# Kernel optimization log

Hardware: AMD Instinct MI355X
Metric: run time of the kernel (lower is better)

## Reference

```python
import jax, jax.numpy as jnp
import numpy as np

BATCH = 2048
INPUT_DIM = 512
N = 8 ** 4  # reservoir_n ** reservoir_d = 4096
T = 16
NEG_SLOPE = 0.1
SPARSITY = 0.1  # fraction of nonzero entries in the pre-trained reservoir W


def setup_inputs() -> dict:
    key = jax.random.key(0)
    kx, kw, km = jax.random.split(key, 3)
    x = jax.random.normal(kx, (BATCH, INPUT_DIM), dtype=jnp.float32)
    # Sparse pre-trained reservoir weights; scale keeps spectral norm ~O(1)
    # so the T-step recurrence neither explodes nor vanishes.
    mask = (jax.random.uniform(km, (N, N)) < SPARSITY).astype(jnp.float32)
    W = jax.random.normal(kw, (N, N), dtype=jnp.float32) * mask / jnp.sqrt(SPARSITY * N)
    return {"x": x, "W": W}


def reference(x, W):
    # Pad input [B, input_dim] -> initial state S [B, N]
    S0 = jnp.pad(x, ((0, 0), (0, N - x.shape[1])))

    def step(S, _):
        S = jax.nn.leaky_relu(S @ W, negative_slope=NEG_SLOPE)
        return S, None

    S_final, _ = jax.lax.scan(step, S0, None, length=T)
    return S_final
```

## Files before the change

kernel.cpp:

```cpp
#include <hip/hip_runtime.h>


#define BATCH 2048
#define NDIM  4096
#define INDIM 512
#define BM 128
#define BN 128
#define BK 32

typedef _Float16 f16x8 __attribute__((ext_vector_type(8)));
typedef float    f32x4 __attribute__((ext_vector_type(4)));

__device__ __forceinline__ void async16(const void* gsrc, void* ldst) {
  const __attribute__((address_space(1))) unsigned int* g =
      (const __attribute__((address_space(1))) unsigned int*)gsrc;
  __attribute__((address_space(3))) unsigned int* l =
      (__attribute__((address_space(3))) unsigned int*)ldst;
  __builtin_amdgcn_global_load_lds(g, l, 16, 0, 0);
}

__device__ __forceinline__ f16x8 frag(const _Float16* s, int row, int q) {
  int ch = q ^ ((row >> 1) & 3);
  return *(const f16x8*)(s + row * BK + ch * 8);
}

__global__ void prep_x(const float* __restrict__ x,
                       _Float16* __restrict__ Sh, _Float16* __restrict__ Sl) {
  size_t i = (size_t)blockIdx.x * 256 + threadIdx.x;
  int b = (int)(i >> 12);
  int n = (int)(i & (NDIM - 1));
  float v = (n < INDIM) ? x[(size_t)b * INDIM + n] : 0.0f;
  _Float16 h = (_Float16)v;
  Sh[i] = h;
  Sl[i] = (_Float16)(v - (float)h);
}

__global__ void prep_w(const float* __restrict__ W,
                       _Float16* __restrict__ Wth, _Float16* __restrict__ Wtl) {
  __shared__ float tile[32][33];
  int k0 = blockIdx.y * 32, n0 = blockIdx.x * 32;
  int tx = threadIdx.x, ty = threadIdx.y;
  for (int r = 0; r < 4; r++) {
    int k = k0 + ty + r * 8;
    tile[ty + r * 8][tx] = W[(size_t)k * NDIM + n0 + tx];
  }
  __syncthreads();
  for (int r = 0; r < 4; r++) {
    int n = n0 + ty + r * 8;
    float v = tile[tx][ty + r * 8] * 256.0f;
    _Float16 h = (_Float16)v;
    Wth[(size_t)n * NDIM + k0 + tx] = h;
    Wtl[(size_t)n * NDIM + k0 + tx] = (_Float16)(v - (float)h);
  }
}

template <int MODE>
__global__ __launch_bounds__(256, 2) void step_kernel(
    const _Float16* __restrict__ Ah, const _Float16* __restrict__ Al,
    const _Float16* __restrict__ Bh, const _Float16* __restrict__ Bl,
    _Float16* __restrict__ Dh, _Float16* __restrict__ Dl,
    float* __restrict__ Dout, int k_len) {
  __shared__ _Float16 sAh[BM * BK];
  __shared__ _Float16 sAl[BM * BK];
  __shared__ _Float16 sBh[BN * BK];
  __shared__ _Float16 sBl[BN * BK];

  const int tid = threadIdx.x;
  const int lane = tid & 63;
  const int w = tid >> 6;
  const int wm = w >> 1;
  const int wn = w & 1;
  const int bm = blockIdx.y * BM;
  const int bn = blockIdx.x * BN;

  const int sr = lane >> 2;
  const int cl = lane & 3;
  const int fm = lane & 15;
  const int fq = lane >> 4;

  f32x4 acc[4][4];
  for (int i = 0; i < 4; i++)
    for (int j = 0; j < 4; j++) acc[i][j] = (f32x4){0.f, 0.f, 0.f, 0.f};

  for (int kt = 0; kt < k_len; kt += BK) {
    for (int q = 0; q < 2; q++) {
      int t = w * 2 + q;
      int r = t * 16 + sr;
      int cg = cl ^ ((r >> 1) & 3);
      size_t goA = (size_t)(bm + r) * NDIM + kt + cg * 8;
      size_t goB = (size_t)(bn + r) * NDIM + kt + cg * 8;
      int lo = r * BK + cl * 8;
      async16(Ah + goA, sAh + lo);
      async16(Al + goA, sAl + lo);
      async16(Bh + goB, sBh + lo);
      async16(Bl + goB, sBl + lo);
    }
    asm volatile("s_waitcnt vmcnt(0)" ::: "memory");
    __syncthreads();

    f16x8 ah[4], al[4];
    for (int i = 0; i < 4; i++) {
      int r = wm * 64 + i * 16 + fm;
      ah[i] = frag(sAh, r, fq);
      al[i] = frag(sAl, r, fq);
    }
    for (int j = 0; j < 4; j++) {
      int r = wn * 64 + j * 16 + fm;
      f16x8 bh = frag(sBh, r, fq);
      f16x8 bl = frag(sBl, r, fq);
      for (int i = 0; i < 4; i++) {
        acc[i][j] = __builtin_amdgcn_mfma_f32_16x16x32_f16(ah[i], bh, acc[i][j], 0, 0, 0);
        acc[i][j] = __builtin_amdgcn_mfma_f32_16x16x32_f16(al[i], bh, acc[i][j], 0, 0, 0);
        acc[i][j] = __builtin_amdgcn_mfma_f32_16x16x32_f16(ah[i], bl, acc[i][j], 0, 0, 0);
      }
    }
    __syncthreads();
  }

  const float inv = 1.0f / 256.0f;
  for (int i = 0; i < 4; i++) {
    for (int j = 0; j < 4; j++) {
      for (int e = 0; e < 4; e++) {
        int r = bm + wm * 64 + i * 16 + fq * 4 + e;
        int c = bn + wn * 64 + j * 16 + fm;
        float g = acc[i][j][e] * inv;
        float s = (g > 0.0f) ? g : 0.1f * g;
        if (MODE == 0) {
          _Float16 h = (_Float16)s;
          Dh[(size_t)r * NDIM + c] = h;
          Dl[(size_t)r * NDIM + c] = (_Float16)(s - (float)h);
        } else {
          Dout[(size_t)r * NDIM + c] = s;
        }
      }
    }
  }
}

extern "C" void kernel_launch(void* const* d_in, const int* in_sizes, int n_in,
                              void* d_out, int out_size, void* d_ws, size_t ws_size,
                              hipStream_t stream) {
  const float* x = (const float*)d_in[0];
  const float* W = (const float*)d_in[1];
  float* out = (float*)d_out;
  char* ws = (char*)d_ws;

  const size_t WT_BYTES = (size_t)NDIM * NDIM * 2;
  const size_t S_BYTES = (size_t)BATCH * NDIM * 2;
  _Float16* Wth = (_Float16*)ws;
  _Float16* Wtl = (_Float16*)(ws + WT_BYTES);
  _Float16* SAh = (_Float16*)(ws + 2 * WT_BYTES);
  _Float16* SAl = (_Float16*)(ws + 2 * WT_BYTES + S_BYTES);
  _Float16* SBh = (_Float16*)(ws + 2 * WT_BYTES + 2 * S_BYTES);
  _Float16* SBl = (_Float16*)(ws + 2 * WT_BYTES + 3 * S_BYTES);

  prep_x<<<(BATCH * NDIM) / 256, 256, 0, stream>>>(x, SAh, SAl);
  prep_w<<<dim3(NDIM / 32, NDIM / 32), dim3(32, 8), 0, stream>>>(W, Wth, Wtl);

  dim3 grid(NDIM / BN, BATCH / BM);
  for (int t = 1; t <= 16; t++) {
    const _Float16* ah = (t & 1) ? SAh : SBh;
    const _Float16* al = (t & 1) ? SAl : SBl;
    _Float16* dh = (t & 1) ? SBh : SAh;
    _Float16* dl = (t & 1) ? SBl : SAl;
    int klen = (t == 1) ? INDIM : NDIM;
    if (t < 16)
      step_kernel<0><<<grid, 256, 0, stream>>>(ah, al, Wth, Wtl, dh, dl, nullptr, klen);
    else
      step_kernel<1><<<grid, 256, 0, stream>>>(ah, al, Wth, Wtl, nullptr, nullptr, out, klen);
  }
}
```

Baseline: 2.674 ms.

## Double-buffer LDS tiles and remap blocks for XCD-local L2 reuse

Splits each shared-memory tile into two buffers so the async global-to-LDS loads for the next K slice are issued before the MFMAs on the current slice, overlapping memory latency with compute. It also flattens the grid to 1D and remaps block IDs so that each of the 8 XCDs handles a contiguous 8x8 group of output tiles, improving L2 reuse of the A and B rows. Doubling LDS to 64KB per block may cut occupancy below the two blocks per CU requested by the launch bounds. The remap hardcodes 512 blocks and an 8-XCD round-robin assignment.

After: 2.683 ms. No clear change (+0.3%).

```diff
diff --git a/kernel.cpp b/kernel.cpp
--- a/kernel.cpp
+++ b/kernel.cpp
@@ -60,18 +60,26 @@
     const _Float16* __restrict__ Bh, const _Float16* __restrict__ Bl,
     _Float16* __restrict__ Dh, _Float16* __restrict__ Dl,
     float* __restrict__ Dout, int k_len) {
-  __shared__ _Float16 sAh[BM * BK];
-  __shared__ _Float16 sAl[BM * BK];
-  __shared__ _Float16 sBh[BN * BK];
-  __shared__ _Float16 sBl[BN * BK];
+  __shared__ _Float16 sAh[2][BM * BK];
+  __shared__ _Float16 sAl[2][BM * BK];
+  __shared__ _Float16 sBh[2][BN * BK];
+  __shared__ _Float16 sBl[2][BN * BK];
 
   const int tid = threadIdx.x;
   const int lane = tid & 63;
   const int w = tid >> 6;
   const int wm = w >> 1;
   const int wn = w & 1;
-  const int bm = blockIdx.y * BM;
-  const int bn = blockIdx.x * BN;
+
+  int id = blockIdx.x;
+  int xcd = id & 7;
+  int local = id >> 3;
+  int lr = local & 7;
+  int lc = local >> 3;
+  int rb = (xcd & 1) * 8 + lr;
+  int cb = (xcd >> 1) * 8 + lc;
+  const int bm = rb * BM;
+  const int bn = cb * BN;
 
   const int sr = lane >> 2;
   const int cl = lane & 3;
@@ -82,7 +90,7 @@
   for (int i = 0; i < 4; i++)
     for (int j = 0; j < 4; j++) acc[i][j] = (f32x4){0.f, 0.f, 0.f, 0.f};
 
-  for (int kt = 0; kt < k_len; kt += BK) {
+  auto stage = [&](int kt, int buf) {
     for (int q = 0; q < 2; q++) {
       int t = w * 2 + q;
       int r = t * 16 + sr;
@@ -90,30 +98,40 @@
       size_t goA = (size_t)(bm + r) * NDIM + kt + cg * 8;
       size_t goB = (size_t)(bn + r) * NDIM + kt + cg * 8;
       int lo = r * BK + cl * 8;
-      async16(Ah + goA, sAh + lo);
-      async16(Al + goA, sAl + lo);
-      async16(Bh + goB, sBh + lo);
-      async16(Bl + goB, sBl + lo);
+      async16(Ah + goA, &sAh[buf][lo]);
+      async16(Al + goA, &sAl[buf][lo]);
+      async16(Bh + goB, &sBh[buf][lo]);
+      async16(Bl + goB, &sBl[buf][lo]);
     }
-    asm volatile("s_waitcnt vmcnt(0)" ::: "memory");
-    __syncthreads();
+  };
+
+  stage(0, 0);
+  asm volatile("s_waitcnt vmcnt(0)" ::: "memory");
+  __syncthreads();
+
+  const int nk = k_len / BK;
+  for (int it = 0; it < nk; it++) {
+    const int cur = it & 1;
+    if (it + 1 < nk) stage((it + 1) * BK, cur ^ 1);
 
     f16x8 ah[4], al[4];
     for (int i = 0; i < 4; i++) {
       int r = wm * 64 + i * 16 + fm;
-      ah[i] = frag(sAh, r, fq);
-      al[i] = frag(sAl, r, fq);
+      ah[i] = frag(sAh[cur], r, fq);
+      al[i] = frag(sAl[cur], r, fq);
     }
     for (int j = 0; j < 4; j++) {
       int r = wn * 64 + j * 16 + fm;
-      f16x8 bh = frag(sBh, r, fq);
-      f16x8 bl = frag(sBl, r, fq);
+      f16x8 bh = frag(sBh[cur], r, fq);
+      f16x8 bl = frag(sBl[cur], r, fq);
       for (int i = 0; i < 4; i++) {
         acc[i][j] = __builtin_amdgcn_mfma_f32_16x16x32_f16(ah[i], bh, acc[i][j], 0, 0, 0);
         acc[i][j] = __builtin_amdgcn_mfma_f32_16x16x32_f16(al[i], bh, acc[i][j], 0, 0, 0);
         acc[i][j] = __builtin_amdgcn_mfma_f32_16x16x32_f16(ah[i], bl, acc[i][j], 0, 0, 0);
       }
     }
+
+    asm volatile("s_waitcnt vmcnt(0)" ::: "memory");
     __syncthreads();
   }
 
@@ -157,7 +175,7 @@
   prep_x<<<(BATCH * NDIM) / 256, 256, 0, stream>>>(x, SAh, SAl);
   prep_w<<<dim3(NDIM / 32, NDIM / 32), dim3(32, 8), 0, stream>>>(W, Wth, Wtl);
 
-  dim3 grid(NDIM / BN, BATCH / BM);
+  dim3 grid((NDIM / BN) * (BATCH / BM));
   for (int t = 1; t <= 16; t++) {
     const _Float16* ah = (t & 1) ? SAh : SBh;
     const _Float16* al = (t & 1) ? SAl : SBl;
```
